# Kernel optimization log

Measured on AMD Instinct MI355X. Metric: run time of the kernel, lower is better.

## Reference

```python
import jax, jax.numpy as jnp
import numpy as np

TEMP = 0.1  # gumbel-softmax temperature hardcoded in forward


def setup_inputs() -> dict:
    key = jax.random.key(0)
    kx, k1, k2, kw, kb = jax.random.split(key, 5)
    B, D_IN, D_OUT = 16384, 1024, 1024
    x = jax.random.normal(kx, (B, D_IN), dtype=jnp.float32)
    # host-side np.random.uniform noise modeled as uniform inputs in (0,1)
    eps = 1e-7
    u1 = jax.random.uniform(k1, (B, D_OUT), dtype=jnp.float32, minval=eps, maxval=1.0 - eps)
    u2 = jax.random.uniform(k2, (B, D_OUT), dtype=jnp.float32, minval=eps, maxval=1.0 - eps)
    W = jax.random.normal(kw, (D_OUT, D_IN), dtype=jnp.float32) * (1.0 / np.sqrt(D_IN))
    b = jax.random.normal(kb, (D_OUT,), dtype=jnp.float32) * 0.01
    return {"x": x, "u1": u1, "u2": u2, "W": W, "b": b, "with_grad": 1}


def reference(x, u1, u2, W, b, with_grad):
    # l = Linear(x); p = sigmoid(l)
    l = jnp.einsum("bi,oi->bo", x, W) + b  # [B, D_OUT]
    # gumbel noise: -log(-log(u))
    g1 = -jnp.log(-jnp.log(u1))
    g2 = -jnp.log(-jnp.log(u2))
    # binary gumbel-softmax:
    #   y1 = exp((log p + g1)/T); y2 = exp((log(1-p) + g2)/T); out = y1/(y1+y2)
    # numerically stable identical form: sigmoid(((log p + g1) - (log(1-p) + g2))/T)
    # and log p - log(1-p) = l (logit), so:
    out = jax.nn.sigmoid((l + g1 - g2) / TEMP)
    return out.astype(jnp.float32)
```

## Files before the change

kernel.cpp:

```cpp
#include <hip/hip_runtime.h>

#define BM 128
#define BN 128
#define BK 64

typedef __attribute__((ext_vector_type(8))) _Float16 half8;
typedef __attribute__((ext_vector_type(2))) __fp16 h2raw;
typedef __attribute__((ext_vector_type(4))) float floatx4;
typedef __attribute__((ext_vector_type(4))) float f4;

#define AS1U(p) ((const __attribute__((address_space(1))) unsigned int*)(p))
#define AS3U(p) ((__attribute__((address_space(3))) unsigned int*)(p))

__global__ __launch_bounds__(256) void cvt_fp32_fp16_2(
        const float* __restrict__ x, _Float16* __restrict__ xh, int nx8,
        const float* __restrict__ W, _Float16* __restrict__ wh, int nw8,
        int xblocks) {
    const f4* s4;
    half8* d8;
    int n8, i, stride;
    if ((int)blockIdx.x < xblocks) {
        s4 = (const f4*)x; d8 = (half8*)xh; n8 = nx8;
        i = blockIdx.x * blockDim.x + threadIdx.x;
        stride = xblocks * blockDim.x;
    } else {
        s4 = (const f4*)W; d8 = (half8*)wh; n8 = nw8;
        i = (blockIdx.x - xblocks) * blockDim.x + threadIdx.x;
        stride = (gridDim.x - xblocks) * blockDim.x;
    }
    union { h2raw h2[4]; half8 h8; } u;
    for (; i < n8; i += stride) {
        f4 a = s4[2 * i];
        f4 b = s4[2 * i + 1];
        u.h2[0] = __builtin_amdgcn_cvt_pkrtz(a.x, a.y);
        u.h2[1] = __builtin_amdgcn_cvt_pkrtz(a.z, a.w);
        u.h2[2] = __builtin_amdgcn_cvt_pkrtz(b.x, b.y);
        u.h2[3] = __builtin_amdgcn_cvt_pkrtz(b.z, b.w);
        d8[i] = u.h8;
    }
}

__global__ __launch_bounds__(256, 4) void gumbel_fused(
        const _Float16* __restrict__ xh, const _Float16* __restrict__ wh,
        const float* __restrict__ bias, const float* __restrict__ u1,
        const float* __restrict__ u2, float* __restrict__ out,
        int M, int N, int K) {
    __shared__ _Float16 Smem[2 * BM * BK];
    _Float16* As = Smem;
    _Float16* Bs = Smem + BM * BK;

    const int tid  = threadIdx.x;
    const int lane = tid & 63;
    const int wave = tid >> 6;

    const int bid = blockIdx.x;
    const int by  = bid & (M / BM - 1);
    const int bx  = bid >> 7;
    const int bm = by * BM;
    const int bn = bx * BN;

    int aoff[4], boff[4], lsoff[4];
#pragma unroll
    for (int rep = 0; rep < 4; rep++) {
        int s = wave * 64 + lane + rep * 256;
        int r = s >> 3;
        int cc = (s & 7) ^ (r & 7);
        aoff[rep] = (bm + r) * K + cc * 8;
        boff[rep] = (bn + r) * K + cc * 8;
        lsoff[rep] = s * 8;
    }

    const int r16  = lane & 15;
    const int quad = lane >> 4;
    const int wm = (wave & 1) * 64;
    const int wn = (wave >> 1) * 64;

    floatx4 acc[4][4] = {};

    int aro[4][2], bro[4][2];
#pragma unroll
    for (int i = 0; i < 4; i++) {
        int ra = wm + i * 16 + r16;
        int rb = wn + i * 16 + r16;
#pragma unroll
        for (int s = 0; s < 2; s++) {
            aro[i][s] = ra * BK + (((s * 4 + quad) ^ (ra & 7)) * 8);
            bro[i][s] = rb * BK + (((s * 4 + quad) ^ (rb & 7)) * 8);
        }
    }

    for (int kb = 0; kb < K; kb += BK) {
#pragma unroll
        for (int rep = 0; rep < 4; rep++) {
            __builtin_amdgcn_global_load_lds(AS1U(xh + aoff[rep] + kb), AS3U(As + lsoff[rep]), 16, 0, 0);
            __builtin_amdgcn_global_load_lds(AS1U(wh + boff[rep] + kb), AS3U(Bs + lsoff[rep]), 16, 0, 0);
        }
        __syncthreads();

#pragma unroll
        for (int s = 0; s < 2; s++) {
            half8 af[4], bf[4];
#pragma unroll
            for (int i = 0; i < 4; i++) {
                af[i] = *(const half8*)(As + aro[i][s]);
                bf[i] = *(const half8*)(Bs + bro[i][s]);
            }
#pragma unroll
            for (int i = 0; i < 4; i++) {
#pragma unroll
                for (int j = 0; j < 4; j++) {
                    acc[i][j] = __builtin_amdgcn_mfma_f32_16x16x32_f16(af[i], bf[j], acc[i][j], 0, 0, 0);
                }
            }
        }
        __syncthreads();
    }

    float* T = ((float*)Smem) + wave * 1280;
    const float inv_t = 10.0f;

#pragma unroll
    for (int i = 0; i < 4; i++) {
#pragma unroll
        for (int j = 0; j < 4; j++) {
            int col = j * 16 + r16;
            f4 v = {acc[i][j][0], acc[i][j][1], acc[i][j][2], acc[i][j][3]};
            *(f4*)(T + col * 20 + quad * 4) = v;
        }
        __syncthreads();

#pragma unroll
        for (int rep = 0; rep < 2; rep++) {
#pragma unroll
            for (int rep2 = 0; rep2 < 2; rep2++) {
                int rr = (lane >> 3) + rep * 8;
                int ch = (lane & 7) + rep2 * 8;
                int gm = bm + wm + i * 16 + rr;
                int gc = bn + wn + ch * 4;
                f4 l4;
                l4.x = T[(ch * 4 + 0) * 20 + rr];
                l4.y = T[(ch * 4 + 1) * 20 + rr];
                l4.z = T[(ch * 4 + 2) * 20 + rr];
                l4.w = T[(ch * 4 + 3) * 20 + rr];
                f4 bv = *(const f4*)(bias + gc);
                int idx = gm * N + gc;
                f4 v1 = __builtin_nontemporal_load((const f4*)(u1 + idx));
                f4 v2 = __builtin_nontemporal_load((const f4*)(u2 + idx));
                f4 o;
                {
                    float z = (l4.x + bv.x + __logf(__logf(v2.x) / __logf(v1.x))) * inv_t;
                    o.x = 1.0f / (1.0f + __expf(-z));
                }
                {
                    float z = (l4.y + bv.y + __logf(__logf(v2.y) / __logf(v1.y))) * inv_t;
                    o.y = 1.0f / (1.0f + __expf(-z));
                }
                {
                    float z = (l4.z + bv.z + __logf(__logf(v2.z) / __logf(v1.z))) * inv_t;
                    o.z = 1.0f / (1.0f + __expf(-z));
                }
                {
                    float z = (l4.w + bv.w + __logf(__logf(v2.w) / __logf(v1.w))) * inv_t;
                    o.w = 1.0f / (1.0f + __expf(-z));
                }
                __builtin_nontemporal_store(o, (f4*)(out + idx));
            }
        }
        __syncthreads();
    }
}

extern "C" void kernel_launch(void* const* d_in, const int* in_sizes, int n_in,
                              void* d_out, int out_size, void* d_ws, size_t ws_size,
                              hipStream_t stream) {
    const float* x  = (const float*)d_in[0];
    const float* u1 = (const float*)d_in[1];
    const float* u2 = (const float*)d_in[2];
    const float* W  = (const float*)d_in[3];
    const float* b  = (const float*)d_in[4];
    float* out = (float*)d_out;

    const int N = in_sizes[4];
    const int K = in_sizes[3] / N;
    const int M = in_sizes[0] / K;

    _Float16* xh = (_Float16*)d_ws;
    _Float16* wh = xh + (size_t)M * K;

    const int xblocks = 2048, wblocks = 256;
    cvt_fp32_fp16_2<<<xblocks + wblocks, 256, 0, stream>>>(
        x, xh, (M * K) / 8, W, wh, (N * K) / 8, xblocks);

    dim3 grid((M / BM) * (N / BN));
    gumbel_fused<<<grid, 256, 0, stream>>>(xh, wh, b, u1, u2, out, M, N, K);
}
```

Before: 254.6 us.

## Pipeline GEMM with triple-buffered LDS, larger 256x128 tiles, and XCD-aware block mapping

```diff
diff --git a/kernel.cpp b/kernel.cpp
--- a/kernel.cpp
+++ b/kernel.cpp
@@ -1,8 +1,11 @@
 #include <hip/hip_runtime.h>
 
-#define BM 128
+#define BM 256
 #define BN 128
 #define BK 64
+#define ASZ (BM * BK)
+#define BSZ (BN * BK)
+#define SLOT (ASZ + BSZ)
 
 typedef __attribute__((ext_vector_type(8))) _Float16 half8;
 typedef __attribute__((ext_vector_type(2))) __fp16 h2raw;
@@ -40,42 +43,50 @@
     }
 }
 
-__global__ __launch_bounds__(256, 4) void gumbel_fused(
+__global__ __launch_bounds__(512, 2) void gumbel_fused(
         const _Float16* __restrict__ xh, const _Float16* __restrict__ wh,
         const float* __restrict__ bias, const float* __restrict__ u1,
         const float* __restrict__ u2, float* __restrict__ out,
         int M, int N, int K) {
-    __shared__ _Float16 Smem[2 * BM * BK];
-    _Float16* As = Smem;
-    _Float16* Bs = Smem + BM * BK;
+    __shared__ _Float16 Smem[3 * SLOT];
 
     const int tid  = threadIdx.x;
     const int lane = tid & 63;
     const int wave = tid >> 6;
 
+    const int nbx = N / BN;
     const int bid = blockIdx.x;
-    const int by  = bid & (M / BM - 1);
-    const int bx  = bid >> 7;
-    const int bm = by * BM;
-    const int bn = bx * BN;
-
-    int aoff[4], boff[4], lsoff[4];
+    const int per = gridDim.x >> 3;
+    const int vid = (bid & 7) * per + (bid >> 3);
+    const int by  = vid / nbx;
+    const int bx  = vid - by * nbx;
+    const int bm  = by * BM;
+    const int bn  = bx * BN;
+
+    int aoff[4], lsA[4], boff[2], lsB[2];
 #pragma unroll
     for (int rep = 0; rep < 4; rep++) {
-        int s = wave * 64 + lane + rep * 256;
+        int s = rep * 512 + tid;
         int r = s >> 3;
         int cc = (s & 7) ^ (r & 7);
         aoff[rep] = (bm + r) * K + cc * 8;
+        lsA[rep] = s * 8;
+    }
+#pragma unroll
+    for (int rep = 0; rep < 2; rep++) {
+        int s = rep * 512 + tid;
+        int r = s >> 3;
+        int cc = (s & 7) ^ (r & 7);
         boff[rep] = (bn + r) * K + cc * 8;
-        lsoff[rep] = s * 8;
+        lsB[rep] = s * 8;
     }
 
     const int r16  = lane & 15;
     const int quad = lane >> 4;
-    const int wm = (wave & 1) * 64;
-    const int wn = (wave >> 1) * 64;
-
-    floatx4 acc[4][4] = {};
+    const int wr = wave >> 1;
+    const int wc = wave & 1;
+    const int wm = wr * 64;
+    const int wn = wc * 64;
 
     int aro[4][2], bro[4][2];
 #pragma unroll
@@ -89,31 +100,65 @@
         }
     }
 
-    for (int kb = 0; kb < K; kb += BK) {
-#pragma unroll
-        for (int rep = 0; rep < 4; rep++) {
-            __builtin_amdgcn_global_load_lds(AS1U(xh + aoff[rep] + kb), AS3U(As + lsoff[rep]), 16, 0, 0);
-            __builtin_amdgcn_global_load_lds(AS1U(wh + boff[rep] + kb), AS3U(Bs + lsoff[rep]), 16, 0, 0);
-        }
-        __syncthreads();
-
-#pragma unroll
-        for (int s = 0; s < 2; s++) {
-            half8 af[4], bf[4];
-#pragma unroll
-            for (int i = 0; i < 4; i++) {
-                af[i] = *(const half8*)(As + aro[i][s]);
-                bf[i] = *(const half8*)(Bs + bro[i][s]);
+    floatx4 acc[4][4] = {};
+    const int KT = K / BK;
+
+#pragma unroll
+    for (int t0 = 0; t0 < 2; t0++) {
+        _Float16* Ap = Smem + t0 * SLOT;
+        _Float16* Bp = Ap + ASZ;
+        int kb = t0 * BK;
+#pragma unroll
+        for (int rep = 0; rep < 4; rep++)
+            __builtin_amdgcn_global_load_lds(AS1U(xh + aoff[rep] + kb), AS3U(Ap + lsA[rep]), 16, 0, 0);
+#pragma unroll
+        for (int rep = 0; rep < 2; rep++)
+            __builtin_amdgcn_global_load_lds(AS1U(wh + boff[rep] + kb), AS3U(Bp + lsB[rep]), 16, 0, 0);
+    }
+
+    int sc = 0;
+    for (int t = 0; t < KT; t++) {
+        {
+            int tp = (t + 2 < KT) ? (t + 2) : (KT - 1);
+            int sp = sc + 2; if (sp >= 3) sp -= 3;
+            _Float16* Ap = Smem + sp * SLOT;
+            _Float16* Bp = Ap + ASZ;
+            int kb = tp * BK;
+#pragma unroll
+            for (int rep = 0; rep < 4; rep++)
+                __builtin_amdgcn_global_load_lds(AS1U(xh + aoff[rep] + kb), AS3U(Ap + lsA[rep]), 16, 0, 0);
+#pragma unroll
+            for (int rep = 0; rep < 2; rep++)
+                __builtin_amdgcn_global_load_lds(AS1U(wh + boff[rep] + kb), AS3U(Bp + lsB[rep]), 16, 0, 0);
+        }
+        asm volatile("s_waitcnt vmcnt(12)" ::: "memory");
+        __builtin_amdgcn_sched_barrier(0);
+        __builtin_amdgcn_s_barrier();
+
+        const _Float16* As = Smem + sc * SLOT;
+        const _Float16* Bs = As + ASZ;
+
+        half8 bf[4][2];
+#pragma unroll
+        for (int j = 0; j < 4; j++)
+#pragma unroll
+            for (int s = 0; s < 2; s++)
+                bf[j][s] = *(const half8*)(Bs + bro[j][s]);
+#pragma unroll
+        for (int i = 0; i < 4; i++) {
+            half8 a0 = *(const half8*)(As + aro[i][0]);
+            half8 a1 = *(const half8*)(As + aro[i][1]);
+            __builtin_amdgcn_s_setprio(1);
+#pragma unroll
+            for (int j = 0; j < 4; j++) {
+                acc[i][j] = __builtin_amdgcn_mfma_f32_16x16x32_f16(a0, bf[j][0], acc[i][j], 0, 0, 0);
+                acc[i][j] = __builtin_amdgcn_mfma_f32_16x16x32_f16(a1, bf[j][1], acc[i][j], 0, 0, 0);
             }
-#pragma unroll
-            for (int i = 0; i < 4; i++) {
-#pragma unroll
-                for (int j = 0; j < 4; j++) {
-                    acc[i][j] = __builtin_amdgcn_mfma_f32_16x16x32_f16(af[i], bf[j], acc[i][j], 0, 0, 0);
-                }
-            }
-        }
-        __syncthreads();
+            __builtin_amdgcn_s_setprio(0);
+        }
+        __builtin_amdgcn_sched_barrier(0);
+        __builtin_amdgcn_s_barrier();
+        sc = sc + 1; if (sc >= 3) sc -= 3;
     }
 
     float* T = ((float*)Smem) + wave * 1280;
@@ -121,14 +166,14 @@
 
 #pragma unroll
     for (int i = 0; i < 4; i++) {
+        asm volatile("s_waitcnt lgkmcnt(0)" ::: "memory");
+        __builtin_amdgcn_sched_barrier(0);
 #pragma unroll
         for (int j = 0; j < 4; j++) {
             int col = j * 16 + r16;
             f4 v = {acc[i][j][0], acc[i][j][1], acc[i][j][2], acc[i][j][3]};
             *(f4*)(T + col * 20 + quad * 4) = v;
         }
-        __syncthreads();
-
 #pragma unroll
         for (int rep = 0; rep < 2; rep++) {
 #pragma unroll
@@ -166,7 +211,6 @@
                 __builtin_nontemporal_store(o, (f4*)(out + idx));
             }
         }
-        __syncthreads();
     }
 }
 
@@ -192,5 +236,5 @@
         x, xh, (M * K) / 8, W, wh, (N * K) / 8, xblocks);
 
     dim3 grid((M / BM) * (N / BN));
-    gumbel_fused<<<grid, 256, 0, stream>>>(xh, wh, b, u1, u2, out, M, N, K);
+    gumbel_fused<<<grid, 512, 0, stream>>>(xh, wh, b, u1, u2, out, M, N, K);
 }
```

Measured after the change: 269.1 us. 5.7% more time.

## Prefetch gumbel noise during last K-step and double-buffer epilogue loads

Applied to the files above, without the earlier changes.

```diff
diff --git a/kernel.cpp b/kernel.cpp
--- a/kernel.cpp
+++ b/kernel.cpp
@@ -40,7 +40,7 @@
     }
 }
 
-__global__ __launch_bounds__(256, 4) void gumbel_fused(
+__global__ __launch_bounds__(256, 3) void gumbel_fused(
         const _Float16* __restrict__ xh, const _Float16* __restrict__ wh,
         const float* __restrict__ bias, const float* __restrict__ u1,
         const float* __restrict__ u2, float* __restrict__ out,
@@ -89,7 +89,24 @@
         }
     }
 
-    for (int kb = 0; kb < K; kb += BK) {
+    const int rrb = lane >> 3;
+    const int chb = lane & 7;
+    const int colA = bn + wn + chb * 4;
+    const f4 bv0 = *(const f4*)(bias + colA);
+    const f4 bv1 = *(const f4*)(bias + colA + 32);
+
+#define NT_LOAD(p) __builtin_nontemporal_load((const f4*)(p))
+#define ISSUE(g, P) do { \
+        int r0_ = (bm + wm + (g) * 16 + rrb) * N + colA; \
+        P##v1[0] = NT_LOAD(u1 + r0_);              P##v2[0] = NT_LOAD(u2 + r0_); \
+        P##v1[1] = NT_LOAD(u1 + r0_ + 32);         P##v2[1] = NT_LOAD(u2 + r0_ + 32); \
+        P##v1[2] = NT_LOAD(u1 + r0_ + 8 * N);      P##v2[2] = NT_LOAD(u2 + r0_ + 8 * N); \
+        P##v1[3] = NT_LOAD(u1 + r0_ + 8 * N + 32); P##v2[3] = NT_LOAD(u2 + r0_ + 8 * N + 32); \
+    } while (0)
+
+    f4 pAv1[4], pAv2[4], pBv1[4], pBv2[4];
+
+    for (int kb = 0; kb < K - BK; kb += BK) {
 #pragma unroll
         for (int rep = 0; rep < 4; rep++) {
             __builtin_amdgcn_global_load_lds(AS1U(xh + aoff[rep] + kb), AS3U(As + lsoff[rep]), 16, 0, 0);
@@ -116,58 +133,97 @@
         __syncthreads();
     }
 
+    {
+        const int kb = K - BK;
+#pragma unroll
+        for (int rep = 0; rep < 4; rep++) {
+            __builtin_amdgcn_global_load_lds(AS1U(xh + aoff[rep] + kb), AS3U(As + lsoff[rep]), 16, 0, 0);
+            __builtin_amdgcn_global_load_lds(AS1U(wh + boff[rep] + kb), AS3U(Bs + lsoff[rep]), 16, 0, 0);
+        }
+        __builtin_amdgcn_sched_barrier(0);
+        ISSUE(0, pA);
+        __builtin_amdgcn_sched_barrier(0);
+        asm volatile("s_waitcnt vmcnt(8)" ::: "memory");
+        __builtin_amdgcn_sched_barrier(0);
+        __builtin_amdgcn_s_barrier();
+
+#pragma unroll
+        for (int s = 0; s < 2; s++) {
+            half8 af[4], bf[4];
+#pragma unroll
+            for (int i = 0; i < 4; i++) {
+                af[i] = *(const half8*)(As + aro[i][s]);
+                bf[i] = *(const half8*)(Bs + bro[i][s]);
+            }
+#pragma unroll
+            for (int i = 0; i < 4; i++) {
+#pragma unroll
+                for (int j = 0; j < 4; j++) {
+                    acc[i][j] = __builtin_amdgcn_mfma_f32_16x16x32_f16(af[i], bf[j], acc[i][j], 0, 0, 0);
+                }
+            }
+        }
+        __builtin_amdgcn_sched_barrier(0);
+        ISSUE(1, pB);
+        __builtin_amdgcn_sched_barrier(0);
+        __builtin_amdgcn_s_barrier();
+    }
+
     float* T = ((float*)Smem) + wave * 1280;
     const float inv_t = 10.0f;
 
-#pragma unroll
-    for (int i = 0; i < 4; i++) {
-#pragma unroll
-        for (int j = 0; j < 4; j++) {
-            int col = j * 16 + r16;
-            f4 v = {acc[i][j][0], acc[i][j][1], acc[i][j][2], acc[i][j][3]};
-            *(f4*)(T + col * 20 + quad * 4) = v;
-        }
-        __syncthreads();
-
-#pragma unroll
-        for (int rep = 0; rep < 2; rep++) {
-#pragma unroll
-            for (int rep2 = 0; rep2 < 2; rep2++) {
-                int rr = (lane >> 3) + rep * 8;
-                int ch = (lane & 7) + rep2 * 8;
-                int gm = bm + wm + i * 16 + rr;
-                int gc = bn + wn + ch * 4;
-                f4 l4;
-                l4.x = T[(ch * 4 + 0) * 20 + rr];
-                l4.y = T[(ch * 4 + 1) * 20 + rr];
-                l4.z = T[(ch * 4 + 2) * 20 + rr];
-                l4.w = T[(ch * 4 + 3) * 20 + rr];
-                f4 bv = *(const f4*)(bias + gc);
-                int idx = gm * N + gc;
-                f4 v1 = __builtin_nontemporal_load((const f4*)(u1 + idx));
-                f4 v2 = __builtin_nontemporal_load((const f4*)(u2 + idx));
-                f4 o;
-                {
-                    float z = (l4.x + bv.x + __logf(__logf(v2.x) / __logf(v1.x))) * inv_t;
-                    o.x = 1.0f / (1.0f + __expf(-z));
-                }
-                {
-                    float z = (l4.y + bv.y + __logf(__logf(v2.y) / __logf(v1.y))) * inv_t;
-                    o.y = 1.0f / (1.0f + __expf(-z));
-                }
-                {
-                    float z = (l4.z + bv.z + __logf(__logf(v2.z) / __logf(v1.z))) * inv_t;
-                    o.z = 1.0f / (1.0f + __expf(-z));
-                }
-                {
-                    float z = (l4.w + bv.w + __logf(__logf(v2.w) / __logf(v1.w))) * inv_t;
-                    o.w = 1.0f / (1.0f + __expf(-z));
-                }
-                __builtin_nontemporal_store(o, (f4*)(out + idx));
-            }
-        }
-        __syncthreads();
-    }
+#define GM1(OC, LC, BC, V1, V2) do { \
+        float a1_ = __logf(V1); \
+        float a2_ = __logf(V2); \
+        float z_  = (LC + BC + __logf(a2_ * __builtin_amdgcn_rcpf(a1_))) * inv_t; \
+        OC = __builtin_amdgcn_rcpf(1.0f + __expf(-z_)); \
+    } while (0)
+
+#define PROCESS(g, P) do { \
+         \
+        asm volatile("s_waitcnt lgkmcnt(0)" ::: "memory"); \
+        __builtin_amdgcn_sched_barrier(0); \
+        _Pragma("unroll") \
+        for (int j = 0; j < 4; j++) { \
+            int col = j * 16 + r16; \
+            f4 v = {acc[g][j][0], acc[g][j][1], acc[g][j][2], acc[g][j][3]}; \
+            *(f4*)(T + col * 20 + quad * 4) = v; \
+        } \
+        _Pragma("unroll") \
+        for (int c = 0; c < 4; c++) { \
+            int rr = rrb + (c >> 1) * 8; \
+            int ch = chb + (c & 1) * 8; \
+            f4 l4; \
+            l4.x = T[(ch * 4 + 0) * 20 + rr]; \
+            l4.y = T[(ch * 4 + 1) * 20 + rr]; \
+            l4.z = T[(ch * 4 + 2) * 20 + rr]; \
+            l4.w = T[(ch * 4 + 3) * 20 + rr]; \
+            f4 bv = (c & 1) ? bv1 : bv0; \
+            int idx = (bm + wm + (g) * 16 + rr) * N + bn + wn + ch * 4; \
+            f4 o; \
+            GM1(o.x, l4.x, bv.x, P##v1[c].x, P##v2[c].x); \
+            GM1(o.y, l4.y, bv.y, P##v1[c].y, P##v2[c].y); \
+            GM1(o.z, l4.z, bv.z, P##v1[c].z, P##v2[c].z); \
+            GM1(o.w, l4.w, bv.w, P##v1[c].w, P##v2[c].w); \
+            __builtin_nontemporal_store(o, (f4*)(out + idx)); \
+        } \
+    } while (0)
+
+    PROCESS(0, pA);
+    __builtin_amdgcn_sched_barrier(0);
+    ISSUE(2, pA);
+    __builtin_amdgcn_sched_barrier(0);
+    PROCESS(1, pB);
+    __builtin_amdgcn_sched_barrier(0);
+    ISSUE(3, pB);
+    __builtin_amdgcn_sched_barrier(0);
+    PROCESS(2, pA);
+    PROCESS(3, pB);
+
+#undef PROCESS
+#undef GM1
+#undef ISSUE
+#undef NT_LOAD
 }
 
 extern "C" void kernel_launch(void* const* d_in, const int* in_sizes, int n_in,
```

Measured after the change: 258.3 us. No clear change (+1.4%).
